# Performance work log

Hardware: AMD Instinct MI355X
Metric: run time of the kernel (lower is better)

The kernel has to match this reference:

```python
import jax, jax.numpy as jnp
import numpy as np

N, C, F, NB = 256, 4, 256, 32   # batch, in_channels, in_features, neighbors
OC, OF = 4, 256                 # out_channels, out_features


def setup_inputs() -> dict:
    key = jax.random.key(0)
    k1, k2, k3 = jax.random.split(key, 3)
    x = jax.random.normal(k1, (N, C, F), dtype=jnp.float32)
    neighbor = jax.random.normal(k2, (N, NB, C, F), dtype=jnp.float32)
    # Conv1d(in=2C, out=OC*OF, kernel_size=F, bias=False) weight
    W = jax.random.normal(k3, (OC * OF, 2 * C, F), dtype=jnp.float32) * 0.02
    return {"x": x, "neighbor": neighbor, "W": W}


def _feature_adjacency(x, neighbor):
    # batched version of per-sample einsum('ca,ncb->cab')
    fadj = jnp.einsum('Nca,Nncb->Ncab', x, neighbor)  # (N,C,F,F)
    fadj = fadj + jnp.swapaxes(fadj, -2, -1)
    # sign-sqrt
    s = jnp.sign(fadj) * jnp.sqrt(jnp.clip(jnp.abs(fadj), 1e-8, None))
    # row(col)-normalize over dim -2, then NaN mask
    adj = s / (jnp.abs(s).sum(-2, keepdims=True) + 1e-7)
    return jnp.where(jnp.isnan(adj), 0.0, adj)


def reference(x, neighbor, W):
    adj = _feature_adjacency(x, neighbor)            # (N,C,F,F)
    ax = jnp.einsum('Ncab,Ncb->Nca', adj, x)         # adj @ x
    xcat = jnp.concatenate([ax, x], axis=1)          # (N,2C,F)
    # Conv1d with kernel_size=F over length-F input == flat contraction
    out = jnp.einsum('Nif,oif->No', xcat, W).reshape(x.shape[0], OC, OF)
    return (out, adj)
```

## Files before the change

kernel.cpp:

```cpp
#include <hip/hip_runtime.h>
#include <math.h>

namespace {
constexpr int N_ = 256, C_ = 4, F_ = 256, NB_ = 32;
constexpr int K_ = 2048;
constexpr int O_ = 1024;
constexpr int OUT_ELEMS = N_ * O_;
}

__global__ __launch_bounds__(256) void adj_kernel(
    const float* __restrict__ x,
    const float* __restrict__ neighbor,
    float* __restrict__ adj,
    float* __restrict__ ax_out)
{
  __shared__ float x_l[F_], s_l[F_], w_l[F_];
  const int blk = blockIdx.x;
  const int n = blk >> 2, c = blk & 3;
  const int b = threadIdx.x;

  const float xb = x[(n * C_ + c) * F_ + b];
  x_l[b] = xb;
  const float* nb_ptr = neighbor + ((size_t)(n * NB_) * C_ + c) * F_ + b;
  float sb = 0.f;
  #pragma unroll
  for (int j = 0; j < NB_; ++j) sb += nb_ptr[(size_t)j * C_ * F_];
  s_l[b] = sb;
  __syncthreads();

  float colsum = 0.f;
  #pragma unroll 8
  for (int a = 0; a < F_; ++a) {
    float v = fmaf(x_l[a], sb, xb * s_l[a]);
    float r = __builtin_amdgcn_sqrtf(fmaxf(fabsf(v), 1e-8f));
    colsum += (v != 0.f) ? r : 0.f;
  }
  const float inv = 1.f / (colsum + 1e-7f);
  w_l[b] = inv * xb;
  __syncthreads();

  float axb = 0.f;
  float* adj_col = adj + (size_t)(n * C_ + c) * F_ * F_ + b;
  #pragma unroll 4
  for (int a = 0; a < F_; ++a) {
    float v = fmaf(x_l[a], sb, xb * s_l[a]);
    float r = __builtin_amdgcn_sqrtf(fmaxf(fabsf(v), 1e-8f));
    float t = (v != 0.f) ? copysignf(r, v) : 0.f;
    adj_col[(size_t)a * F_] = t * inv;
    axb = fmaf(t, w_l[a], axb);
  }
  ax_out[(n * C_ + c) * F_ + b] = axb;
}

__global__ __launch_bounds__(64) void gemm_kernel(
    const float* __restrict__ ax,
    const float* __restrict__ x,
    const float* __restrict__ W,
    float* __restrict__ out)
{
  __shared__ float As[32][36];
  __shared__ float Bs[32][36];
  const int m0 = blockIdx.x * 32;
  const int o0 = blockIdx.y * 32;
  const int kb = blockIdx.z;
  const int lane = threadIdx.x;
  const int lx = lane & 7, ly = lane >> 3;

  float acc[4][4] = {};
  const int kbeg = kb * 256;
  for (int k0 = kbeg; k0 < kbeg + 256; k0 += 32) {
    const float* Abase = (k0 < 1024) ? (ax + k0) : (x + (k0 - 1024));
    #pragma unroll
    for (int i = 0; i < 16; ++i) {
      int idx = i * 64 + lane;
      int r = idx >> 5, kk = idx & 31;
      As[r][kk] = Abase[(size_t)(m0 + r) * 1024 + kk];
      Bs[r][kk] = W[(size_t)(o0 + r) * 2048 + k0 + kk];
    }
    __syncthreads();
    #pragma unroll
    for (int kk = 0; kk < 32; ++kk) {
      float a4[4], b4[4];
      #pragma unroll
      for (int i = 0; i < 4; ++i) a4[i] = As[ly * 4 + i][kk];
      #pragma unroll
      for (int j = 0; j < 4; ++j) b4[j] = Bs[lx * 4 + j][kk];
      #pragma unroll
      for (int i = 0; i < 4; ++i)
        #pragma unroll
        for (int j = 0; j < 4; ++j)
          acc[i][j] = fmaf(a4[i], b4[j], acc[i][j]);
    }
    __syncthreads();
  }
  #pragma unroll
  for (int i = 0; i < 4; ++i)
    #pragma unroll
    for (int j = 0; j < 4; ++j)
      atomicAdd(&out[(size_t)(m0 + ly * 4 + i) * 1024 + o0 + lx * 4 + j],
                acc[i][j]);
}

extern "C" void kernel_launch(void* const* d_in, const int* in_sizes, int n_in,
                              void* d_out, int out_size, void* d_ws,
                              size_t ws_size, hipStream_t stream) {
  const float* x = (const float*)d_in[0];
  const float* neighbor = (const float*)d_in[1];
  const float* W = (const float*)d_in[2];
  float* out = (float*)d_out;
  float* adj = out + OUT_ELEMS;
  float* ax = (float*)d_ws;

  hipMemsetAsync(out, 0, OUT_ELEMS * sizeof(float), stream);

  adj_kernel<<<dim3(N_ * C_), dim3(256), 0, stream>>>(x, neighbor, adj, ax);
  gemm_kernel<<<dim3(N_ / 32, O_ / 32, 8), dim3(64), 0, stream>>>(ax, x, W,
                                                                  out);
}
```

Before: 351.8 us.

## Vectorize adjacency row stores and retile GEMM to 64x64 blocks

The adjacency kernel now gives each thread four consecutive columns and splits the rows across four wavefronts. Column sums and ax are reduced through shared memory, and the adj output is written as contiguous float4 nontemporal stores instead of strided scalar stores. The GEMM grows from 32x32 tiles with 64 threads to 64x64 tiles with 256 threads, uses vectorized global loads, and stores k-major transposed tiles so the inner loop can read float4 from shared memory. This adds shared-memory reductions and extra barriers, and the transposed shared stores may hit bank conflicts.

```diff
diff --git a/kernel.cpp b/kernel.cpp
--- a/kernel.cpp
+++ b/kernel.cpp
@@ -3,9 +3,9 @@
 
 namespace {
 constexpr int N_ = 256, C_ = 4, F_ = 256, NB_ = 32;
-constexpr int K_ = 2048;
 constexpr int O_ = 1024;
 constexpr int OUT_ELEMS = N_ * O_;
+typedef float f32x4 __attribute__((ext_vector_type(4)));
 }
 
 __global__ __launch_bounds__(256) void adj_kernel(
@@ -15,89 +15,143 @@
     float* __restrict__ ax_out)
 {
   __shared__ float x_l[F_], s_l[F_], w_l[F_];
+  __shared__ float red[4][F_];
   const int blk = blockIdx.x;
   const int n = blk >> 2, c = blk & 3;
-  const int b = threadIdx.x;
+  const int t = threadIdx.x;
+  const int rs = t >> 6;
+  const int lane = t & 63;
+  const int b0 = lane * 4;
 
-  const float xb = x[(n * C_ + c) * F_ + b];
-  x_l[b] = xb;
-  const float* nb_ptr = neighbor + ((size_t)(n * NB_) * C_ + c) * F_ + b;
-  float sb = 0.f;
-  #pragma unroll
-  for (int j = 0; j < NB_; ++j) sb += nb_ptr[(size_t)j * C_ * F_];
-  s_l[b] = sb;
+  const int base = (n * C_ + c) * F_;
+  x_l[t] = x[base + t];
+  {
+    const float* p = neighbor + ((size_t)(n * NB_) * C_ + c) * F_ + t;
+    float s = 0.f;
+    #pragma unroll
+    for (int j = 0; j < NB_; ++j) s += p[(size_t)j * C_ * F_];
+    s_l[t] = s;
+  }
   __syncthreads();
 
-  float colsum = 0.f;
-  #pragma unroll 8
-  for (int a = 0; a < F_; ++a) {
-    float v = fmaf(x_l[a], sb, xb * s_l[a]);
-    float r = __builtin_amdgcn_sqrtf(fmaxf(fabsf(v), 1e-8f));
-    colsum += (v != 0.f) ? r : 0.f;
+  const float4 xb4 = *(const float4*)&x_l[b0];
+  const float4 sb4 = *(const float4*)&s_l[b0];
+  const float xbv[4] = {xb4.x, xb4.y, xb4.z, xb4.w};
+  const float sbv[4] = {sb4.x, sb4.y, sb4.z, sb4.w};
+
+  float cs[4] = {0.f, 0.f, 0.f, 0.f};
+  const int a0r = rs * 64;
+  #pragma unroll 4
+  for (int a = a0r; a < a0r + 64; ++a) {
+    const float xa = x_l[a], sa = s_l[a];
+    #pragma unroll
+    for (int j = 0; j < 4; ++j) {
+      float v = fmaf(xa, sbv[j], xbv[j] * sa);
+      float r = __builtin_amdgcn_sqrtf(fmaxf(fabsf(v), 1e-8f));
+      cs[j] += (v != 0.f) ? r : 0.f;
+    }
   }
-  const float inv = 1.f / (colsum + 1e-7f);
-  w_l[b] = inv * xb;
+  *(float4*)&red[rs][b0] = make_float4(cs[0], cs[1], cs[2], cs[3]);
   __syncthreads();
 
-  float axb = 0.f;
-  float* adj_col = adj + (size_t)(n * C_ + c) * F_ * F_ + b;
-  #pragma unroll 4
-  for (int a = 0; a < F_; ++a) {
-    float v = fmaf(x_l[a], sb, xb * s_l[a]);
-    float r = __builtin_amdgcn_sqrtf(fmaxf(fabsf(v), 1e-8f));
-    float t = (v != 0.f) ? copysignf(r, v) : 0.f;
-    adj_col[(size_t)a * F_] = t * inv;
-    axb = fmaf(t, w_l[a], axb);
+  float invv[4];
+  {
+    const float4 r0 = *(const float4*)&red[0][b0];
+    const float4 r1 = *(const float4*)&red[1][b0];
+    const float4 r2 = *(const float4*)&red[2][b0];
+    const float4 r3 = *(const float4*)&red[3][b0];
+    invv[0] = 1.f / (r0.x + r1.x + r2.x + r3.x + 1e-7f);
+    invv[1] = 1.f / (r0.y + r1.y + r2.y + r3.y + 1e-7f);
+    invv[2] = 1.f / (r0.z + r1.z + r2.z + r3.z + 1e-7f);
+    invv[3] = 1.f / (r0.w + r1.w + r2.w + r3.w + 1e-7f);
   }
-  ax_out[(n * C_ + c) * F_ + b] = axb;
+  if (rs == 0) {
+    *(float4*)&w_l[b0] = make_float4(invv[0] * xbv[0], invv[1] * xbv[1],
+                                     invv[2] * xbv[2], invv[3] * xbv[3]);
+  }
+  __syncthreads();
+
+  float axp[4] = {0.f, 0.f, 0.f, 0.f};
+  float* arow = adj + (size_t)(n * C_ + c) * (F_ * F_);
+  #pragma unroll 2
+  for (int a = a0r; a < a0r + 64; ++a) {
+    const float xa = x_l[a], sa = s_l[a], wa = w_l[a];
+    float o[4];
+    #pragma unroll
+    for (int j = 0; j < 4; ++j) {
+      float v = fmaf(xa, sbv[j], xbv[j] * sa);
+      float r = __builtin_amdgcn_sqrtf(fmaxf(fabsf(v), 1e-8f));
+      float tt = (v != 0.f) ? copysignf(r, v) : 0.f;
+      o[j] = tt * invv[j];
+      axp[j] = fmaf(tt, wa, axp[j]);
+    }
+    f32x4 ov = {o[0], o[1], o[2], o[3]};
+    __builtin_nontemporal_store(ov, (f32x4*)&arow[(size_t)a * F_ + b0]);
+  }
+  *(float4*)&red[rs][b0] = make_float4(axp[0], axp[1], axp[2], axp[3]);
+  __syncthreads();
+  if (rs == 0) {
+    const float4 r0 = *(const float4*)&red[0][b0];
+    const float4 r1 = *(const float4*)&red[1][b0];
+    const float4 r2 = *(const float4*)&red[2][b0];
+    const float4 r3 = *(const float4*)&red[3][b0];
+    const float4 axv = make_float4(r0.x + r1.x + r2.x + r3.x,
+                                   r0.y + r1.y + r2.y + r3.y,
+                                   r0.z + r1.z + r2.z + r3.z,
+                                   r0.w + r1.w + r2.w + r3.w);
+    *(float4*)&ax_out[base + b0] = axv;
+  }
 }
 
-__global__ __launch_bounds__(64) void gemm_kernel(
+__global__ __launch_bounds__(256) void gemm_kernel(
     const float* __restrict__ ax,
     const float* __restrict__ x,
     const float* __restrict__ W,
     float* __restrict__ out)
 {
-  __shared__ float As[32][36];
-  __shared__ float Bs[32][36];
-  const int m0 = blockIdx.x * 32;
-  const int o0 = blockIdx.y * 32;
-  const int kb = blockIdx.z;
-  const int lane = threadIdx.x;
-  const int lx = lane & 7, ly = lane >> 3;
+  __shared__ float As[32][64];
+  __shared__ float Bs[32][64];
+  const int tid = threadIdx.x;
+  const int m0 = blockIdx.x * 64, o0 = blockIdx.y * 64;
+  const int mi = tid >> 4, oi = tid & 15;
+  const int r = tid >> 2, kq = (tid & 3) * 8;
+  float acc[4][4] = {};
 
-  float acc[4][4] = {};
-  const int kbeg = kb * 256;
+  const int kbeg = blockIdx.z * 256;
   for (int k0 = kbeg; k0 < kbeg + 256; k0 += 32) {
-    const float* Abase = (k0 < 1024) ? (ax + k0) : (x + (k0 - 1024));
-    #pragma unroll
-    for (int i = 0; i < 16; ++i) {
-      int idx = i * 64 + lane;
-      int r = idx >> 5, kk = idx & 31;
-      As[r][kk] = Abase[(size_t)(m0 + r) * 1024 + kk];
-      Bs[r][kk] = W[(size_t)(o0 + r) * 2048 + k0 + kk];
-    }
+    const float* Ab = (k0 < 1024) ? ax + k0 : x + (k0 - 1024);
+    const float4 a0 = *(const float4*)&Ab[(size_t)(m0 + r) * 1024 + kq];
+    const float4 a1 = *(const float4*)&Ab[(size_t)(m0 + r) * 1024 + kq + 4];
+    const float4 b0 = *(const float4*)&W[(size_t)(o0 + r) * 2048 + k0 + kq];
+    const float4 b1 = *(const float4*)&W[(size_t)(o0 + r) * 2048 + k0 + kq + 4];
+    __syncthreads();
+    As[kq + 0][r] = a0.x; As[kq + 1][r] = a0.y;
+    As[kq + 2][r] = a0.z; As[kq + 3][r] = a0.w;
+    As[kq + 4][r] = a1.x; As[kq + 5][r] = a1.y;
+    As[kq + 6][r] = a1.z; As[kq + 7][r] = a1.w;
+    Bs[kq + 0][r] = b0.x; Bs[kq + 1][r] = b0.y;
+    Bs[kq + 2][r] = b0.z; Bs[kq + 3][r] = b0.w;
+    Bs[kq + 4][r] = b1.x; Bs[kq + 5][r] = b1.y;
+    Bs[kq + 6][r] = b1.z; Bs[kq + 7][r] = b1.w;
     __syncthreads();
     #pragma unroll
     for (int kk = 0; kk < 32; ++kk) {
-      float a4[4], b4[4];
-      #pragma unroll
-      for (int i = 0; i < 4; ++i) a4[i] = As[ly * 4 + i][kk];
-      #pragma unroll
-      for (int j = 0; j < 4; ++j) b4[j] = Bs[lx * 4 + j][kk];
+      const float4 av = *(const float4*)&As[kk][mi * 4];
+      const float4 bv = *(const float4*)&Bs[kk][oi * 4];
+      const float am[4] = {av.x, av.y, av.z, av.w};
+      const float bm[4] = {bv.x, bv.y, bv.z, bv.w};
       #pragma unroll
       for (int i = 0; i < 4; ++i)
         #pragma unroll
         for (int j = 0; j < 4; ++j)
-          acc[i][j] = fmaf(a4[i], b4[j], acc[i][j]);
+          acc[i][j] = fmaf(am[i], bm[j], acc[i][j]);
     }
-    __syncthreads();
   }
   #pragma unroll
   for (int i = 0; i < 4; ++i)
     #pragma unroll
     for (int j = 0; j < 4; ++j)
-      atomicAdd(&out[(size_t)(m0 + ly * 4 + i) * 1024 + o0 + lx * 4 + j],
+      atomicAdd(&out[(size_t)(m0 + mi * 4 + i) * 1024 + o0 + oi * 4 + j],
                 acc[i][j]);
 }
 
@@ -111,9 +165,8 @@
   float* adj = out + OUT_ELEMS;
   float* ax = (float*)d_ws;
 
-  hipMemsetAsync(out, 0, OUT_ELEMS * sizeof(float), stream);
-
+  (void)hipMemsetAsync(out, 0, OUT_ELEMS * sizeof(float), stream);
   adj_kernel<<<dim3(N_ * C_), dim3(256), 0, stream>>>(x, neighbor, adj, ax);
-  gemm_kernel<<<dim3(N_ / 32, O_ / 32, 8), dim3(64), 0, stream>>>(ax, x, W,
-                                                                  out);
+  gemm_kernel<<<dim3(256 / 64, O_ / 64, 8), dim3(256), 0, stream>>>(ax, x, W,
+                                                                    out);
 }
```

Result: no change. 345.0 us (-1.9%).
